# Performance work log

Measured on AMD Instinct MI355X. Metric: run time of the kernel, lower is better.

## Reference

```python
import jax, jax.numpy as jnp
import numpy as np

TOPK = 13
NUM_CLASSES = 80
ALPHA = 1.0
BETA = 6.0
EPS = 1e-9


def _ciou(gt, pd, eps=1e-7):
    """CIoU between gt (B,M,1,4) and pd (B,1,N,4) xyxy boxes -> (B,M,N)."""
    g_x1, g_y1, g_x2, g_y2 = (gt[..., i] for i in range(4))
    p_x1, p_y1, p_x2, p_y2 = (pd[..., i] for i in range(4))
    iw = jnp.clip(jnp.minimum(g_x2, p_x2) - jnp.maximum(g_x1, p_x1), 0.0)
    ih = jnp.clip(jnp.minimum(g_y2, p_y2) - jnp.maximum(g_y1, p_y1), 0.0)
    inter = iw * ih
    w1, h1 = g_x2 - g_x1, g_y2 - g_y1 + eps
    w2, h2 = p_x2 - p_x1, p_y2 - p_y1 + eps
    union = w1 * h1 + w2 * h2 - inter + eps
    iou = inter / union
    cw = jnp.maximum(g_x2, p_x2) - jnp.minimum(g_x1, p_x1)  # enclosing box
    ch = jnp.maximum(g_y2, p_y2) - jnp.minimum(g_y1, p_y1)
    c2 = cw * cw + ch * ch + eps
    rho2 = ((p_x1 + p_x2 - g_x1 - g_x2) ** 2 + (p_y1 + p_y2 - g_y1 - g_y2) ** 2) / 4.0
    v = (4.0 / jnp.pi ** 2) * (jnp.arctan(w2 / h2) - jnp.arctan(w1 / h1)) ** 2
    a = jax.lax.stop_gradient(v / (v - iou + (1.0 + eps)))  # torch.no_grad alpha
    return iou - (rho2 / c2 + v * a)


def setup_inputs() -> dict:
    key = jax.random.key(0)
    ks = jax.random.split(key, 7)
    B, N, M, C = 16, 8400, 32, NUM_CLASSES
    pd_scores = jax.random.uniform(ks[0], (B, N, C), dtype=jnp.float32)
    # YOLO-style anchor centers for 640x640, strides 8/16/32 -> 8400 points
    pts = []
    for s in (8, 16, 32):
        g = 640 // s
        xs = (jnp.arange(g, dtype=jnp.float32) + 0.5) * s
        xx, yy = jnp.meshgrid(xs, xs, indexing="xy")
        pts.append(jnp.stack([xx.ravel(), yy.ravel()], axis=-1))
    anc_points = jnp.concatenate(pts, axis=0)  # (8400, 2)
    ctr = anc_points[None] + jax.random.normal(ks[1], (B, N, 2)) * 8.0
    wh = jax.random.uniform(ks[2], (B, N, 2), minval=8.0, maxval=128.0)
    pd_bboxes = jnp.concatenate([ctr - wh / 2, ctr + wh / 2], axis=-1)
    gctr = jax.random.uniform(ks[3], (B, M, 2), minval=32.0, maxval=608.0)
    gwh = jax.random.uniform(ks[4], (B, M, 2), minval=16.0, maxval=256.0)
    gt_bboxes = jnp.concatenate([gctr - gwh / 2, gctr + gwh / 2], axis=-1)
    gt_labels = jax.random.randint(ks[5], (B, M, 1), 0, C)
    counts = jax.random.randint(ks[6], (B, 1), 1, M + 1)
    mask_gt = (jnp.arange(M)[None, :] < counts)[..., None]  # (B, M, 1) bool prefix-valid
    return {"pd_scores": pd_scores, "pd_bboxes": pd_bboxes, "anc_points": anc_points,
            "gt_labels": gt_labels, "gt_bboxes": gt_bboxes, "mask_gt": mask_gt}


def reference(pd_scores, pd_bboxes, anc_points, gt_labels, gt_bboxes, mask_gt):
    B, N, C = pd_scores.shape
    M = gt_bboxes.shape[1]
    mask_gt2 = mask_gt[..., 0]  # (B, M) bool
    # --- anchors whose centers lie inside each GT box ---
    lt = gt_bboxes[:, :, None, :2]  # (B, M, 1, 2)
    rb = gt_bboxes[:, :, None, 2:]
    anc = anc_points[None, None]    # (1, 1, N, 2)
    deltas = jnp.concatenate([anc - lt, rb - anc], axis=-1)  # (B, M, N, 4)
    mask_in_gts = jnp.min(deltas, axis=-1) > 1e-9            # (B, M, N)
    valid = mask_in_gts & mask_gt2[:, :, None]
    # --- alignment metric = score^alpha * ciou^beta (masked) ---
    cls = gt_labels[..., 0]                      # (B, M)
    scores_t = jnp.swapaxes(pd_scores, 1, 2)     # (B, C, N)
    bbox_scores = jnp.where(valid, scores_t[jnp.arange(B)[:, None], cls], 0.0)  # (B, M, N)
    overlaps = jnp.where(valid, jnp.clip(_ciou(gt_bboxes[:, :, None], pd_bboxes[:, None]), 0.0), 0.0)
    align_metric = bbox_scores ** ALPHA * overlaps ** BETA
    # --- top-k candidate anchors per GT ---
    _, topk_idx = jax.lax.top_k(align_metric, TOPK)          # (B, M, TOPK)
    bi = jnp.arange(B)[:, None, None]
    mi = jnp.arange(M)[None, :, None]
    src = jnp.broadcast_to(mask_gt2[:, :, None], topk_idx.shape)
    mask_topk = jnp.zeros((B, M, N), dtype=bool).at[bi, mi, topk_idx].set(src)
    mask_pos = mask_topk & valid                             # (B, M, N)
    # --- resolve anchors claimed by multiple GTs: keep highest CIoU ---
    fg_count = jnp.sum(mask_pos, axis=1)                     # (B, N)
    best_gt = jnp.argmax(overlaps, axis=1)                   # (B, N)
    is_max = jnp.arange(M)[None, :, None] == best_gt[:, None, :]
    mask_pos_f = jnp.where(fg_count[:, None, :] > 1, is_max, mask_pos).astype(pd_scores.dtype)
    fg_mask = jnp.sum(mask_pos_f, axis=1)                    # (B, N) float 0/1
    target_gt_idx = jnp.argmax(mask_pos_f, axis=1)           # (B, N)
    # --- gather targets ---
    brow = jnp.arange(B)[:, None]
    target_labels = cls[brow, target_gt_idx]                 # (B, N)
    target_bboxes = gt_bboxes[brow, target_gt_idx]           # (B, N, 4)
    target_scores = jax.nn.one_hot(target_labels, C, dtype=jnp.float32) * fg_mask[..., None]
    # --- normalize scores by per-GT best metric/overlap ---
    align_metric = align_metric * mask_pos_f
    pos_align = jnp.max(align_metric, axis=-1, keepdims=True)            # (B, M, 1)
    pos_over = jnp.max(overlaps * mask_pos_f, axis=-1, keepdims=True)    # (B, M, 1)
    norm_align = jnp.max(align_metric * pos_over / (pos_align + EPS), axis=1)  # (B, N)
    target_scores = target_scores * norm_align[..., None]
    return target_labels, target_bboxes, target_scores, fg_mask > 0, target_gt_idx
```

## Files before the change

### kernel.cpp

```cpp
#include <hip/hip_runtime.h>
#include <math.h>

#define B_ 16
#define N_ 8400
#define M_ 32
#define C_ 80
#define TOPK_ 13
#define SEG_ 8
#define SEGLEN_ (N_ / SEG_)
#define CAND_ (SEG_ * TOPK_)

__device__ __forceinline__ bool in_gt(double ax, double ay,
    double gx1, double gy1, double gx2, double gy2) {
  return (ax - gx1 > 1e-9) && (ay - gy1 > 1e-9) &&
         (gx2 - ax > 1e-9) && (gy2 - ay > 1e-9);
}

__device__ __forceinline__ double ciou_ov(
    double px1, double py1, double px2, double py2,
    double gx1, double gy1, double gx2, double gy2,
    double atp, double atg) {
  double iw = fmin(gx2, px2) - fmax(gx1, px1); iw = iw > 0.0 ? iw : 0.0;
  double ih = fmin(gy2, py2) - fmax(gy1, py1); ih = ih > 0.0 ? ih : 0.0;
  double inter = iw * ih;
  double w1 = gx2 - gx1, h1 = gy2 - gy1 + 1e-7;
  double w2 = px2 - px1, h2 = py2 - py1 + 1e-7;
  double uni = w1 * h1 + w2 * h2 - inter + 1e-7;
  double iou = inter / uni;
  double cw = fmax(gx2, px2) - fmin(gx1, px1);
  double ch = fmax(gy2, py2) - fmin(gy1, py1);
  double c2 = cw * cw + ch * ch + 1e-7;
  double dx = px1 + px2 - gx1 - gx2, dy = py1 + py2 - gy1 - gy2;
  double rho2 = (dx * dx + dy * dy) * 0.25;
  double dv = atp - atg;
  double v = (4.0 / (M_PI * M_PI)) * dv * dv;
  double a = v / (v - iou + (1.0 + 1e-7));
  double c = iou - (rho2 / c2 + v * a);
  return c > 0.0 ? c : 0.0;
}

__global__ __launch_bounds__(256) void k_prep(
    const float* __restrict__ pd_bboxes, const float* __restrict__ gt_bboxes,
    const unsigned char* __restrict__ raw,
    double* __restrict__ atp, double* __restrict__ atg,
    unsigned char* __restrict__ mask) {
  int gid = blockIdx.x * 256 + threadIdx.x;
  if (gid < B_ * N_) {
    double x1 = pd_bboxes[(size_t)gid * 4 + 0], y1 = pd_bboxes[(size_t)gid * 4 + 1];
    double x2 = pd_bboxes[(size_t)gid * 4 + 2], y2 = pd_bboxes[(size_t)gid * 4 + 3];
    atp[gid] = atan((x2 - x1) / (y2 - y1 + 1e-7));
  }
  if (gid < B_ * M_) {
    double x1 = gt_bboxes[gid * 4 + 0], y1 = gt_bboxes[gid * 4 + 1];
    double x2 = gt_bboxes[gid * 4 + 2], y2 = gt_bboxes[gid * 4 + 3];
    atg[gid] = atan((x2 - x1) / (y2 - y1 + 1e-7));
  }
  if (blockIdx.x == 0) {
    __shared__ int s_bad;
    int t = threadIdx.x;
    if (t == 0) s_bad = 0;
    __syncthreads();
    if (t < B_) {
      int cnt = 0; bool seen0 = false; bool bad = false;
      for (int m = 0; m < M_; ++m) {
        unsigned char v = raw[t * M_ + m];
        if (v > 1) { bad = true; break; }
        if (v) { if (seen0) { bad = true; break; } ++cnt; }
        else seen0 = true;
      }
      if (cnt < 1) bad = true;
      if (bad) atomicOr(&s_bad, 1);
    }
    __syncthreads();
    bool ok = (s_bad == 0);
    const int* ri = (const int*)raw;
    for (int i = t; i < B_ * M_; i += 256)
      mask[i] = ok ? (raw[i] ? 1 : 0) : ((ri[i] != 0) ? 1 : 0);
  }
}

__global__ __launch_bounds__(256) void k_seg(
    const float* __restrict__ pd_scores, const float* __restrict__ pd_bboxes,
    const float* __restrict__ anc, const int* __restrict__ gt_labels,
    const float* __restrict__ gt_bboxes, const unsigned char* __restrict__ mask,
    const double* __restrict__ atp, const double* __restrict__ atg,
    double* __restrict__ SEGV, int* __restrict__ SEGI) {
  int row = blockIdx.y;
  if (!mask[row]) return;
  int seg = blockIdx.x;
  int b = row >> 5;
  int t = threadIdx.x;
  int base = seg * SEGLEN_;

  double gx1 = gt_bboxes[row * 4 + 0], gy1 = gt_bboxes[row * 4 + 1];
  double gx2 = gt_bboxes[row * 4 + 2], gy2 = gt_bboxes[row * 4 + 3];
  double atgm = atg[row];
  int cls = gt_labels[row];

  const float4* pb4 = (const float4*)(pd_bboxes + (size_t)b * N_ * 4);
  const float2* an2 = (const float2*)anc;
  const double* ap  = atp + (size_t)b * N_;
  const float*  scp = pd_scores + (size_t)b * N_ * C_ + cls;

  double tv[TOPK_]; int ti[TOPK_];
#pragma unroll
  for (int j = 0; j < TOPK_; ++j) { tv[j] = -1.0; ti[j] = 0x7fffffff; }

  auto body = [&](int n) {
    float4 pbox = pb4[n];
    double atpn = ap[n];
    float  svc  = scp[(size_t)n * C_];
    float2 a2   = an2[n];
    bool val = in_gt((double)a2.x, (double)a2.y, gx1, gy1, gx2, gy2);
    double am = 0.0;
    if (val) {
      double ov = ciou_ov((double)pbox.x, (double)pbox.y, (double)pbox.z,
                          (double)pbox.w, gx1, gy1, gx2, gy2, atpn, atgm);
      double o2 = ov * ov;
      am = (double)svc * (o2 * o2 * o2);
    }
    if (am > tv[TOPK_ - 1]) {
      double cv = am; int ci = n;
#pragma unroll
      for (int j = 0; j < TOPK_; ++j) {
        bool sw = (cv > tv[j]) || (cv == tv[j] && ci < ti[j]);
        double xv = tv[j]; int xi = ti[j];
        if (sw) { tv[j] = cv; ti[j] = ci; cv = xv; ci = xi; }
      }
    }
  };

#pragma unroll
  for (int it = 0; it < 4; ++it) body(base + t + it * 256);
  if (t < SEGLEN_ - 1024) body(base + 1024 + t);

  __shared__ double sval[TOPK_ * 256];
  __shared__ int    sidx[TOPK_ * 256];
#pragma unroll
  for (int j = 0; j < TOPK_; ++j) { sval[j * 256 + t] = tv[j]; sidx[j * 256 + t] = ti[j]; }

  for (int s = 128; s >= 1; s >>= 1) {
    __syncthreads();
    if (t < s) {
      double ov_[TOPK_]; int oi_[TOPK_];
      int a = 0, bq = 0;
#pragma unroll
      for (int k = 0; k < TOPK_; ++k) {
        double va = sval[a * 256 + t],  vb = sval[bq * 256 + t + s];
        int    ia = sidx[a * 256 + t],  ib = sidx[bq * 256 + t + s];
        bool takeA = (va > vb) || (va == vb && ia < ib);
        ov_[k] = takeA ? va : vb;
        oi_[k] = takeA ? ia : ib;
        if (takeA) ++a; else ++bq;
      }
#pragma unroll
      for (int k = 0; k < TOPK_; ++k) { sval[k * 256 + t] = ov_[k]; sidx[k * 256 + t] = oi_[k]; }
    }
  }
  __syncthreads();

  if (t < TOPK_) {
    size_t o = (size_t)row * CAND_ + seg * TOPK_ + t;
    SEGV[o] = sval[t * 256];
    SEGI[o] = sidx[t * 256];
  }
}

__global__ __launch_bounds__(128) void k_merge(
    const double* __restrict__ SEGV, const int* __restrict__ SEGI,
    const float* __restrict__ anc, const float* __restrict__ gt_bboxes,
    const unsigned char* __restrict__ mask, unsigned int* __restrict__ MPB) {
  int row = blockIdx.x;
  if (!mask[row]) return;
  int b = row >> 5, m = row & 31;
  int t = threadIdx.x;

  __shared__ double s_v[CAND_];
  __shared__ int    s_i[CAND_];
  __shared__ int    s_w[TOPK_];
  if (t < CAND_) {
    s_v[t] = SEGV[(size_t)row * CAND_ + t];
    s_i[t] = SEGI[(size_t)row * CAND_ + t];
  }
  __syncthreads();

  if (t == 0) {
    int p[SEG_];
#pragma unroll
    for (int s = 0; s < SEG_; ++s) p[s] = s * TOPK_;
    for (int k = 0; k < TOPK_; ++k) {
      double bv = -2.0; int bi = 0x7fffffff; int bs = 0;
#pragma unroll
      for (int s = 0; s < SEG_; ++s) {
        if (p[s] < (s + 1) * TOPK_) {
          double v = s_v[p[s]]; int i = s_i[p[s]];
          if (v > bv || (v == bv && i < bi)) { bv = v; bi = i; bs = s; }
        }
      }
      s_w[k] = bi;
      p[bs]++;
    }
  }
  __syncthreads();

  if (t < TOPK_) {
    int n = s_w[t];
    double gx1 = gt_bboxes[row * 4 + 0], gy1 = gt_bboxes[row * 4 + 1];
    double gx2 = gt_bboxes[row * 4 + 2], gy2 = gt_bboxes[row * 4 + 3];
    float2 a2 = ((const float2*)anc)[n];
    if (in_gt((double)a2.x, (double)a2.y, gx1, gy1, gx2, gy2))
      atomicOr(&MPB[(size_t)b * N_ + n], 1u << m);
  }
}

__global__ __launch_bounds__(256) void k_colassign(
    const float* __restrict__ pd_scores, const float* __restrict__ pd_bboxes,
    const float* __restrict__ anc, const int* __restrict__ gt_labels,
    const float* __restrict__ gt_bboxes, const unsigned char* __restrict__ mask,
    const double* __restrict__ atp, const double* __restrict__ atg,
    const unsigned int* __restrict__ MPB,
    unsigned char* __restrict__ TG, unsigned char* __restrict__ FG,
    float* __restrict__ OVC, float* __restrict__ AMC,
    unsigned int* __restrict__ PAL, unsigned int* __restrict__ POV) {
  int b = blockIdx.y;
  int n = blockIdx.x * 256 + threadIdx.x;

  __shared__ float s_g[M_][4];
  __shared__ double s_atg[M_];
  __shared__ int s_cls[M_];
  __shared__ unsigned char s_msk[M_];
  if (threadIdx.x < M_) {
    int gi = b * M_ + threadIdx.x;
    s_g[threadIdx.x][0] = gt_bboxes[gi * 4 + 0];
    s_g[threadIdx.x][1] = gt_bboxes[gi * 4 + 1];
    s_g[threadIdx.x][2] = gt_bboxes[gi * 4 + 2];
    s_g[threadIdx.x][3] = gt_bboxes[gi * 4 + 3];
    s_atg[threadIdx.x] = atg[gi];
    s_cls[threadIdx.x] = gt_labels[gi];
    s_msk[threadIdx.x] = mask[gi];
  }
  __syncthreads();
  if (n >= N_) return;

  size_t i = (size_t)b * N_ + n;
  unsigned int mpb = MPB[i];
  int cnt = __popc(mpb);
  int tg = 0; unsigned char fg = 0;
  double ov = 0.0;

  if (cnt >= 1) {
    fg = 1;
    float2 a2 = ((const float2*)anc)[n];
    float4 pbox = ((const float4*)(pd_bboxes + (size_t)b * N_ * 4))[n];
    double atpn = atp[i];
    if (cnt == 1) {
      tg = __ffs(mpb) - 1;
      double g0 = s_g[tg][0], g1 = s_g[tg][1], g2 = s_g[tg][2], g3 = s_g[tg][3];
      bool val = s_msk[tg] && in_gt((double)a2.x, (double)a2.y, g0, g1, g2, g3);
      ov = val ? ciou_ov((double)pbox.x, (double)pbox.y, (double)pbox.z,
                         (double)pbox.w, g0, g1, g2, g3, atpn, s_atg[tg]) : 0.0;
    } else {
      double best = -1.0;
      for (int mm = 0; mm < M_; ++mm) {
        double g0 = s_g[mm][0], g1 = s_g[mm][1], g2 = s_g[mm][2], g3 = s_g[mm][3];
        bool val = s_msk[mm] && in_gt((double)a2.x, (double)a2.y, g0, g1, g2, g3);
        double o = val ? ciou_ov((double)pbox.x, (double)pbox.y, (double)pbox.z,
                                 (double)pbox.w, g0, g1, g2, g3, atpn, s_atg[mm])
                       : 0.0;
        if (o > best) { best = o; tg = mm; }
      }
      ov = best;
    }
  }

  TG[i] = (unsigned char)tg;
  FG[i] = fg;

  if (fg) {
    double o2 = ov * ov;
    double am = (double)pd_scores[i * C_ + s_cls[tg]] * (o2 * o2 * o2);
    float ovf = (float)ov, amf = (float)am;
    OVC[i] = ovf; AMC[i] = amf;
    atomicMax(&PAL[b * M_ + tg], __float_as_uint(amf));
    atomicMax(&POV[b * M_ + tg], __float_as_uint(ovf));
  }
}

__global__ __launch_bounds__(256) void k_emit(
    const int* __restrict__ gt_labels, const float* __restrict__ gt_bboxes,
    const unsigned char* __restrict__ TG, const unsigned char* __restrict__ FG,
    const float* __restrict__ AMC,
    const unsigned int* __restrict__ PAL, const unsigned int* __restrict__ POV,
    float* __restrict__ out) {
  int b = blockIdx.y;
  int n0 = blockIdx.x * 64;
  int t = threadIdx.x;

  __shared__ float s_g[M_][4];
  __shared__ int s_cls[M_];
  __shared__ float s_pal[M_], s_pov[M_];
  __shared__ float s_na[64];
  __shared__ int   s_lab[64];
  __shared__ int   s_tg[64];
  __shared__ unsigned char s_fg[64];
  if (t < M_) {
    int gi = b * M_ + t;
    s_g[t][0] = gt_bboxes[gi * 4 + 0];
    s_g[t][1] = gt_bboxes[gi * 4 + 1];
    s_g[t][2] = gt_bboxes[gi * 4 + 2];
    s_g[t][3] = gt_bboxes[gi * 4 + 3];
    s_cls[t] = gt_labels[gi];
    s_pal[t] = __uint_as_float(PAL[gi]);
    s_pov[t] = __uint_as_float(POV[gi]);
  }
  __syncthreads();

  if (t < 64) {
    int n = n0 + t;
    if (n < N_) {
      size_t i = (size_t)b * N_ + n;
      int tg = TG[i];
      unsigned char fg = FG[i];
      float na = 0.0f;
      if (fg) {
        double am = (double)AMC[i];
        na = (float)(am * (double)s_pov[tg] / ((double)s_pal[tg] + 1e-9));
      }
      s_na[t] = na; s_lab[t] = s_cls[tg]; s_tg[t] = tg; s_fg[t] = fg;
    }
  }
  __syncthreads();

  float* o0 = out;
  float* o1 = out + (size_t)B_ * N_;
  float* o2 = out + (size_t)B_ * N_ * 5;
  float* o3 = out + (size_t)B_ * N_ * 85;
  float* o4 = out + (size_t)B_ * N_ * 86;

  if (t < 64) {
    int n = n0 + t;
    if (n < N_) {
      size_t i = (size_t)b * N_ + n;
      o0[i] = (float)s_lab[t];
      o3[i] = s_fg[t] ? 1.0f : 0.0f;
      o4[i] = (float)s_tg[t];
      int tg = s_tg[t];
      ((float4*)o1)[i] = make_float4(s_g[tg][0], s_g[tg][1], s_g[tg][2], s_g[tg][3]);
    }
  }

#pragma unroll
  for (int k = 0; k < 5; ++k) {
    int id = t + k * 256;
    int a = id / 20, j = id % 20;
    int n = n0 + a;
    if (n < N_) {
      int lab = s_lab[a];
      float na = s_fg[a] ? s_na[a] : 0.0f;
      int c0 = 4 * j;
      float4 w;
      w.x = (c0 + 0 == lab) ? na : 0.0f;
      w.y = (c0 + 1 == lab) ? na : 0.0f;
      w.z = (c0 + 2 == lab) ? na : 0.0f;
      w.w = (c0 + 3 == lab) ? na : 0.0f;
      ((float4*)(o2 + ((size_t)b * N_ + n) * C_))[j] = w;
    }
  }
}

extern "C" void kernel_launch(void* const* d_in, const int* in_sizes, int n_in,
                              void* d_out, int out_size, void* d_ws, size_t ws_size,
                              hipStream_t stream) {
  const float* pd_scores = (const float*)d_in[0];
  const float* pd_bboxes = (const float*)d_in[1];
  const float* anc       = (const float*)d_in[2];
  const int*   gt_labels = (const int*)d_in[3];
  const float* gt_bboxes = (const float*)d_in[4];
  const unsigned char* mask_raw = (const unsigned char*)d_in[5];

  char* ws = (char*)d_ws;
  size_t off = 0;
  double* ATP = (double*)(ws + off); off += (size_t)B_ * N_ * 8;
  double* ATG = (double*)(ws + off); off += (size_t)B_ * M_ * 8;
  double* SEGV = (double*)(ws + off); off += (size_t)B_ * M_ * CAND_ * 8;
  int*    SEGI = (int*)(ws + off);    off += (size_t)B_ * M_ * CAND_ * 4;
  unsigned int* MPB = (unsigned int*)(ws + off); size_t z0 = off; off += (size_t)B_ * N_ * 4;
  unsigned int* PAL = (unsigned int*)(ws + off); off += (size_t)B_ * M_ * 4;
  unsigned int* POV = (unsigned int*)(ws + off); off += (size_t)B_ * M_ * 4;
  size_t zlen = off - z0;
  unsigned char* TG   = (unsigned char*)(ws + off); off += (size_t)B_ * N_;
  unsigned char* FG   = (unsigned char*)(ws + off); off += (size_t)B_ * N_;
  float* OVC = (float*)(ws + off); off += (size_t)B_ * N_ * 4;
  float* AMC = (float*)(ws + off); off += (size_t)B_ * N_ * 4;
  unsigned char* MASK = (unsigned char*)(ws + off); off += (size_t)B_ * M_;

  hipMemsetAsync(ws + z0, 0, zlen, stream);

  k_prep<<<(B_ * N_ + 255) / 256, 256, 0, stream>>>(pd_bboxes, gt_bboxes,
                                                    mask_raw, ATP, ATG, MASK);
  dim3 gseg(SEG_, B_ * M_);
  k_seg<<<gseg, 256, 0, stream>>>(pd_scores, pd_bboxes, anc, gt_labels,
                                  gt_bboxes, MASK, ATP, ATG, SEGV, SEGI);
  k_merge<<<B_ * M_, 128, 0, stream>>>(SEGV, SEGI, anc, gt_bboxes, MASK, MPB);
  dim3 gbn((N_ + 255) / 256, B_);
  k_colassign<<<gbn, 256, 0, stream>>>(pd_scores, pd_bboxes, anc, gt_labels,
                                       gt_bboxes, MASK, ATP, ATG, MPB,
                                       TG, FG, OVC, AMC, PAL, POV);
  dim3 gem((N_ + 63) / 64, B_);
  k_emit<<<gem, 256, 0, stream>>>(gt_labels, gt_bboxes, TG, FG, AMC, PAL, POV,
                                  (float*)d_out);
}
```

Measured before the change: 196.3 us.

## Fuse segmented top-k and merge into one per-row kernel with wave-shuffle bitonic merge

Replaces the 8-segment top-k kernel plus separate merge kernel with a single block per GT row that scans all anchors, then merges per-thread top-16 lists via xor-shuffle bitonic merges and a final 4-wave merge in one thread. Box, atan and score loads are now done only for anchors inside the GT box. Also drops the unused OVC write. This removes the intermediate global buffers and one launch, and it drops the shared-memory tree reduction. The cost is 8x fewer blocks, with each thread doing 33 iterations, and heavier register use from 16-entry double lists.

```diff
diff --git a/kernel.cpp b/kernel.cpp
--- a/kernel.cpp
+++ b/kernel.cpp
@@ -6,9 +6,7 @@
 #define M_ 32
 #define C_ 80
 #define TOPK_ 13
-#define SEG_ 8
-#define SEGLEN_ (N_ / SEG_)
-#define CAND_ (SEG_ * TOPK_)
+#define KL_ 16
 
 __device__ __forceinline__ bool in_gt(double ax, double ay,
     double gx1, double gy1, double gx2, double gy2) {
@@ -39,6 +37,31 @@
   return c > 0.0 ? c : 0.0;
 }
 
+#define MERGE_LISTS(av, ai, bv, bi)                                          \
+  {                                                                          \
+    _Pragma("unroll")                                                        \
+    for (int j = 0; j < KL_; ++j) {                                          \
+      double vb = bv[KL_ - 1 - j]; int ib = bi[KL_ - 1 - j];                 \
+      bool take = (vb > av[j]) || (vb == av[j] && ib < ai[j]);               \
+      av[j] = take ? vb : av[j];                                             \
+      ai[j] = take ? ib : ai[j];                                             \
+    }                                                                        \
+    _Pragma("unroll")                                                        \
+    for (int dd = 8; dd >= 1; dd >>= 1) {                                    \
+      _Pragma("unroll")                                                      \
+      for (int j = 0; j < KL_; ++j) {                                        \
+        if (!(j & dd)) {                                                     \
+          int kk = j | dd;                                                   \
+          bool sw = (av[kk] > av[j]) ||                                      \
+                    (av[kk] == av[j] && ai[kk] < ai[j]);                     \
+          double xv = av[j]; int xi = ai[j];                                 \
+          av[j] = sw ? av[kk] : av[j]; ai[j] = sw ? ai[kk] : ai[j];          \
+          av[kk] = sw ? xv : av[kk];   ai[kk] = sw ? xi : ai[kk];            \
+        }                                                                    \
+      }                                                                      \
+    }                                                                        \
+  }
+
 __global__ __launch_bounds__(256) void k_prep(
     const float* __restrict__ pd_bboxes, const float* __restrict__ gt_bboxes,
     const unsigned char* __restrict__ raw,
@@ -79,18 +102,16 @@
   }
 }
 
-__global__ __launch_bounds__(256) void k_seg(
+__global__ __launch_bounds__(256) void k_topk(
     const float* __restrict__ pd_scores, const float* __restrict__ pd_bboxes,
     const float* __restrict__ anc, const int* __restrict__ gt_labels,
     const float* __restrict__ gt_bboxes, const unsigned char* __restrict__ mask,
     const double* __restrict__ atp, const double* __restrict__ atg,
-    double* __restrict__ SEGV, int* __restrict__ SEGI) {
-  int row = blockIdx.y;
+    unsigned int* __restrict__ MPB) {
+  int row = blockIdx.x;
   if (!mask[row]) return;
-  int seg = blockIdx.x;
-  int b = row >> 5;
+  int b = row >> 5, m = row & 31;
   int t = threadIdx.x;
-  int base = seg * SEGLEN_;
 
   double gx1 = gt_bboxes[row * 4 + 0], gy1 = gt_bboxes[row * 4 + 1];
   double gx2 = gt_bboxes[row * 4 + 2], gy2 = gt_bboxes[row * 4 + 3];
@@ -102,22 +123,20 @@
   const double* ap  = atp + (size_t)b * N_;
   const float*  scp = pd_scores + (size_t)b * N_ * C_ + cls;
 
-  double tv[TOPK_]; int ti[TOPK_];
-#pragma unroll
-  for (int j = 0; j < TOPK_; ++j) { tv[j] = -1.0; ti[j] = 0x7fffffff; }
+  double tv[KL_]; int ti[KL_];
+#pragma unroll
+  for (int j = 0; j < KL_; ++j) { tv[j] = -1.0; ti[j] = 0x7fffffff; }
 
   auto body = [&](int n) {
-    float4 pbox = pb4[n];
-    double atpn = ap[n];
-    float  svc  = scp[(size_t)n * C_];
-    float2 a2   = an2[n];
+    float2 a2 = an2[n];
     bool val = in_gt((double)a2.x, (double)a2.y, gx1, gy1, gx2, gy2);
     double am = 0.0;
     if (val) {
+      float4 pbox = pb4[n];
       double ov = ciou_ov((double)pbox.x, (double)pbox.y, (double)pbox.z,
-                          (double)pbox.w, gx1, gy1, gx2, gy2, atpn, atgm);
+                          (double)pbox.w, gx1, gy1, gx2, gy2, ap[n], atgm);
       double o2 = ov * ov;
-      am = (double)svc * (o2 * o2 * o2);
+      am = (double)scp[(size_t)n * C_] * (o2 * o2 * o2);
     }
     if (am > tv[TOPK_ - 1]) {
       double cv = am; int ci = n;
@@ -130,84 +149,47 @@
     }
   };
 
-#pragma unroll
-  for (int it = 0; it < 4; ++it) body(base + t + it * 256);
-  if (t < SEGLEN_ - 1024) body(base + 1024 + t);
-
-  __shared__ double sval[TOPK_ * 256];
-  __shared__ int    sidx[TOPK_ * 256];
-#pragma unroll
-  for (int j = 0; j < TOPK_; ++j) { sval[j * 256 + t] = tv[j]; sidx[j * 256 + t] = ti[j]; }
-
-  for (int s = 128; s >= 1; s >>= 1) {
-    __syncthreads();
-    if (t < s) {
-      double ov_[TOPK_]; int oi_[TOPK_];
-      int a = 0, bq = 0;
-#pragma unroll
-      for (int k = 0; k < TOPK_; ++k) {
-        double va = sval[a * 256 + t],  vb = sval[bq * 256 + t + s];
-        int    ia = sidx[a * 256 + t],  ib = sidx[bq * 256 + t + s];
-        bool takeA = (va > vb) || (va == vb && ia < ib);
-        ov_[k] = takeA ? va : vb;
-        oi_[k] = takeA ? ia : ib;
-        if (takeA) ++a; else ++bq;
-      }
-#pragma unroll
-      for (int k = 0; k < TOPK_; ++k) { sval[k * 256 + t] = ov_[k]; sidx[k * 256 + t] = oi_[k]; }
-    }
+  for (int it = 0; it < 32; ++it) body(t + it * 256);
+  if (t < N_ - 8192) body(t + 8192);
+
+#pragma unroll
+  for (int d = 1; d <= 32; d <<= 1) {
+    double bv[KL_]; int bi[KL_];
+#pragma unroll
+    for (int j = 0; j < KL_; ++j) {
+      bv[j] = __shfl_xor(tv[j], d, 64);
+      bi[j] = __shfl_xor(ti[j], d, 64);
+    }
+    MERGE_LISTS(tv, ti, bv, bi)
+  }
+
+  __shared__ double s_v[4 * KL_];
+  __shared__ int    s_i[4 * KL_];
+  __shared__ int    s_sel[TOPK_];
+  int wave = t >> 6, lane = t & 63;
+  if (lane == 0) {
+#pragma unroll
+    for (int j = 0; j < KL_; ++j) { s_v[wave * KL_ + j] = tv[j]; s_i[wave * KL_ + j] = ti[j]; }
+  }
+  __syncthreads();
+  if (t == 0) {
+    double av[KL_]; int ai[KL_];
+#pragma unroll
+    for (int j = 0; j < KL_; ++j) { av[j] = s_v[j]; ai[j] = s_i[j]; }
+    for (int w = 1; w < 4; ++w) {
+      double bv[KL_]; int bi[KL_];
+#pragma unroll
+      for (int j = 0; j < KL_; ++j) { bv[j] = s_v[w * KL_ + j]; bi[j] = s_i[w * KL_ + j]; }
+      MERGE_LISTS(av, ai, bv, bi)
+    }
+#pragma unroll
+    for (int j = 0; j < TOPK_; ++j) s_sel[j] = ai[j];
   }
   __syncthreads();
 
   if (t < TOPK_) {
-    size_t o = (size_t)row * CAND_ + seg * TOPK_ + t;
-    SEGV[o] = sval[t * 256];
-    SEGI[o] = sidx[t * 256];
-  }
-}
-
-__global__ __launch_bounds__(128) void k_merge(
-    const double* __restrict__ SEGV, const int* __restrict__ SEGI,
-    const float* __restrict__ anc, const float* __restrict__ gt_bboxes,
-    const unsigned char* __restrict__ mask, unsigned int* __restrict__ MPB) {
-  int row = blockIdx.x;
-  if (!mask[row]) return;
-  int b = row >> 5, m = row & 31;
-  int t = threadIdx.x;
-
-  __shared__ double s_v[CAND_];
-  __shared__ int    s_i[CAND_];
-  __shared__ int    s_w[TOPK_];
-  if (t < CAND_) {
-    s_v[t] = SEGV[(size_t)row * CAND_ + t];
-    s_i[t] = SEGI[(size_t)row * CAND_ + t];
-  }
-  __syncthreads();
-
-  if (t == 0) {
-    int p[SEG_];
-#pragma unroll
-    for (int s = 0; s < SEG_; ++s) p[s] = s * TOPK_;
-    for (int k = 0; k < TOPK_; ++k) {
-      double bv = -2.0; int bi = 0x7fffffff; int bs = 0;
-#pragma unroll
-      for (int s = 0; s < SEG_; ++s) {
-        if (p[s] < (s + 1) * TOPK_) {
-          double v = s_v[p[s]]; int i = s_i[p[s]];
-          if (v > bv || (v == bv && i < bi)) { bv = v; bi = i; bs = s; }
-        }
-      }
-      s_w[k] = bi;
-      p[bs]++;
-    }
-  }
-  __syncthreads();
-
-  if (t < TOPK_) {
-    int n = s_w[t];
-    double gx1 = gt_bboxes[row * 4 + 0], gy1 = gt_bboxes[row * 4 + 1];
-    double gx2 = gt_bboxes[row * 4 + 2], gy2 = gt_bboxes[row * 4 + 3];
-    float2 a2 = ((const float2*)anc)[n];
+    int n = s_sel[t];
+    float2 a2 = an2[n];
     if (in_gt((double)a2.x, (double)a2.y, gx1, gy1, gx2, gy2))
       atomicOr(&MPB[(size_t)b * N_ + n], 1u << m);
   }
@@ -220,7 +202,7 @@
     const double* __restrict__ atp, const double* __restrict__ atg,
     const unsigned int* __restrict__ MPB,
     unsigned char* __restrict__ TG, unsigned char* __restrict__ FG,
-    float* __restrict__ OVC, float* __restrict__ AMC,
+    float* __restrict__ AMC,
     unsigned int* __restrict__ PAL, unsigned int* __restrict__ POV) {
   int b = blockIdx.y;
   int n = blockIdx.x * 256 + threadIdx.x;
@@ -280,7 +262,7 @@
     double o2 = ov * ov;
     double am = (double)pd_scores[i * C_ + s_cls[tg]] * (o2 * o2 * o2);
     float ovf = (float)ov, amf = (float)am;
-    OVC[i] = ovf; AMC[i] = amf;
+    AMC[i] = amf;
     atomicMax(&PAL[b * M_ + tg], __float_as_uint(amf));
     atomicMax(&POV[b * M_ + tg], __float_as_uint(ovf));
   }
@@ -382,15 +364,12 @@
   size_t off = 0;
   double* ATP = (double*)(ws + off); off += (size_t)B_ * N_ * 8;
   double* ATG = (double*)(ws + off); off += (size_t)B_ * M_ * 8;
-  double* SEGV = (double*)(ws + off); off += (size_t)B_ * M_ * CAND_ * 8;
-  int*    SEGI = (int*)(ws + off);    off += (size_t)B_ * M_ * CAND_ * 4;
   unsigned int* MPB = (unsigned int*)(ws + off); size_t z0 = off; off += (size_t)B_ * N_ * 4;
   unsigned int* PAL = (unsigned int*)(ws + off); off += (size_t)B_ * M_ * 4;
   unsigned int* POV = (unsigned int*)(ws + off); off += (size_t)B_ * M_ * 4;
   size_t zlen = off - z0;
   unsigned char* TG   = (unsigned char*)(ws + off); off += (size_t)B_ * N_;
   unsigned char* FG   = (unsigned char*)(ws + off); off += (size_t)B_ * N_;
-  float* OVC = (float*)(ws + off); off += (size_t)B_ * N_ * 4;
   float* AMC = (float*)(ws + off); off += (size_t)B_ * N_ * 4;
   unsigned char* MASK = (unsigned char*)(ws + off); off += (size_t)B_ * M_;
 
@@ -398,14 +377,12 @@
 
   k_prep<<<(B_ * N_ + 255) / 256, 256, 0, stream>>>(pd_bboxes, gt_bboxes,
                                                     mask_raw, ATP, ATG, MASK);
-  dim3 gseg(SEG_, B_ * M_);
-  k_seg<<<gseg, 256, 0, stream>>>(pd_scores, pd_bboxes, anc, gt_labels,
-                                  gt_bboxes, MASK, ATP, ATG, SEGV, SEGI);
-  k_merge<<<B_ * M_, 128, 0, stream>>>(SEGV, SEGI, anc, gt_bboxes, MASK, MPB);
+  k_topk<<<B_ * M_, 256, 0, stream>>>(pd_scores, pd_bboxes, anc, gt_labels,
+                                      gt_bboxes, MASK, ATP, ATG, MPB);
   dim3 gbn((N_ + 255) / 256, B_);
   k_colassign<<<gbn, 256, 0, stream>>>(pd_scores, pd_bboxes, anc, gt_labels,
                                        gt_bboxes, MASK, ATP, ATG, MPB,
-                                       TG, FG, OVC, AMC, PAL, POV);
+                                       TG, FG, AMC, PAL, POV);
   dim3 gem((N_ + 63) / 64, B_);
   k_emit<<<gem, 256, 0, stream>>>(gt_labels, gt_bboxes, TG, FG, AMC, PAL, POV,
                                   (float*)d_out);
```

Measured after the change: 176.1 us. 10.3% less time.
